# Kernel optimization log

Measured on AMD Instinct MI355X. Metric: run time of the kernel, lower is better.

## Reference

```python
import jax, jax.numpy as jnp
import numpy as np

NEG_INF = -1e30

def _pool_unpool(x, k):
    # x: [B, C, H, W]. Non-overlapping max pool with window k (floor-mode,
    # matching torch MaxPool2d default), then MaxUnpool: scatter the pooled max
    # back to its argmax location within each window, zeros elsewhere.
    B, C, H, W = x.shape
    Hc, Wc = (H // k) * k, (W // k) * k  # cropped region covered by windows
    xc = x[:, :, :Hc, :Wc]
    # reshape into windows: [B, C, H/k, k, W/k, k] -> [B, C, H/k, W/k, k*k]
    xw = xc.reshape(B, C, Hc // k, k, Wc // k, k).transpose(0, 1, 2, 4, 3, 5)
    xw = xw.reshape(B, C, Hc // k, Wc // k, k * k)
    mx = jnp.max(xw, axis=-1, keepdims=True)
    am = jnp.argmax(xw, axis=-1)  # first max index, matches torch tie-breaking
    onehot = (jnp.arange(k * k) == am[..., None])
    yw = jnp.where(onehot, mx, jnp.zeros_like(mx))
    yc = yw.reshape(B, C, Hc // k, Wc // k, k, k).transpose(0, 1, 2, 4, 3, 5)
    yc = yc.reshape(B, C, Hc, Wc)
    # output_size=size in torch unpool -> pad uncovered border with zeros
    return jnp.pad(yc, ((0, 0), (0, 0), (0, H - Hc), (0, W - Wc)))

def setup_inputs() -> dict:
    key = jax.random.key(0)
    x = jax.random.uniform(key, (16, 1, 1080, 1920), dtype=jnp.float32)
    return {"x": x}

def reference(x):
    k = 3
    x = _pool_unpool(x, k)
    x = _pool_unpool(x, k + 2)
    x = _pool_unpool(x, k + 3)
    return x
```

## Files before the change

kernel.cpp:

```cpp
#include <hip/hip_runtime.h>
#include <stdint.h>


#define IMG_H 1080
#define IMG_W 1920

template <int K>
__device__ __forceinline__ void stage(float (&v)[30], int cg, int cc) {
    constexpr int NW = 30 / K;
#pragma unroll
    for (int j = 0; j < NW; ++j) {
        float vm = v[j * K];
#pragma unroll
        for (int rr = 1; rr < K; ++rr) vm = fmaxf(vm, v[j * K + rr]);
        float M = vm;
#pragma unroll
        for (int q = 0; q < K; ++q) M = fmaxf(M, __shfl(vm, cg + q, 64));
        unsigned mask = 0u;
#pragma unroll
        for (int rr = 0; rr < K; ++rr)
            mask |= (v[j * K + rr] == M) ? (1u << rr) : 0u;
        unsigned comb = 0u, pre = 0u;
#pragma unroll
        for (int q = 0; q < K; ++q) {
            const unsigned mq = (unsigned)__shfl((int)mask, cg + q, 64);
            comb |= mq;
            pre |= (q < cc) ? mq : 0u;
        }
        const int R = __ffs(comb) - 1;
        const bool win = ((mask >> R) & 1u) != 0u && ((pre >> R) & 1u) == 0u;
#pragma unroll
        for (int rr = 0; rr < K; ++rr)
            v[j * K + rr] = (win && rr == R) ? M : 0.0f;
    }
}

__global__ __launch_bounds__(256, 6) void pooling_nms_kernel(
    const float* __restrict__ x, float* __restrict__ out) {
    const int t = threadIdx.x;
    const int w = t >> 6;
    const int lane = t & 63;
    const int c = (lane < 60) ? lane : 59;
    const int col0 = blockIdx.x * 240 + w * 60;
    const size_t base = (size_t)blockIdx.z * (IMG_H * (size_t)IMG_W) +
                        (size_t)(blockIdx.y * 30) * IMG_W + col0 + c;
    const float* src = x + base;
    float* dst = out + base;

    float v[30];
#pragma unroll
    for (int r = 0; r < 30; ++r) v[r] = src[(size_t)r * IMG_W];

    {
        const int cg = (c / 3) * 3;
        stage<3>(v, cg, c - cg);
    }
    {
        const int cg = (c / 5) * 5;
        stage<5>(v, cg, c - cg);
    }
    {
        const int cg = (c / 6) * 6;
        stage<6>(v, cg, c - cg);
    }

    if (lane < 60) {
#pragma unroll
        for (int r = 0; r < 30; ++r) dst[(size_t)r * IMG_W] = v[r];
    }
}

extern "C" void kernel_launch(void* const* d_in, const int* in_sizes, int n_in,
                              void* d_out, int out_size, void* d_ws, size_t ws_size,
                              hipStream_t stream) {
    const float* x = (const float*)d_in[0];
    float* out = (float*)d_out;
    dim3 grid(IMG_W / 240, IMG_H / 30, 16);
    pooling_nms_kernel<<<grid, 256, 0, stream>>>(x, out);
}
```

Before: 241.7 us.

## Stage tile through LDS with direct global-to-LDS 16-byte loads and float4 stores

Global reads now go straight into a shared-memory tile through the global_load_lds builtin, using 16-byte transfers in row-contiguous chunks instead of per-thread strided 4-byte loads. Each thread then reads its column from LDS, runs the three pool/unpool stages in registers, and writes results back to LDS. The tile is then stored to global memory as float4. The aim is wider, better-coalesced memory transactions. In exchange it adds two block barriers and about 30 KB of LDS per block, which may lower occupancy, and the min-blocks launch bound is dropped.

```diff
diff --git a/kernel.cpp b/kernel.cpp
--- a/kernel.cpp
+++ b/kernel.cpp
@@ -4,6 +4,13 @@
 
 #define IMG_H 1080
 #define IMG_W 1920
+#define TH 30
+#define TW 240
+#define LSTRIDE 256
+#define NTHREADS 256
+
+#define GPTR(p) ((const __attribute__((address_space(1))) void*)(p))
+#define LPTR(p) ((__attribute__((address_space(3))) void*)(p))
 
 template <int K>
 __device__ __forceinline__ void stage(float (&v)[30], int cg, int cc) {
@@ -35,21 +42,32 @@
     }
 }
 
-__global__ __launch_bounds__(256, 6) void pooling_nms_kernel(
+__global__ __launch_bounds__(NTHREADS) void pooling_nms_kernel(
     const float* __restrict__ x, float* __restrict__ out) {
+    __shared__ float tile[TH * LSTRIDE];
+
     const int t = threadIdx.x;
     const int w = t >> 6;
     const int lane = t & 63;
     const int c = (lane < 60) ? lane : 59;
-    const int col0 = blockIdx.x * 240 + w * 60;
+
     const size_t base = (size_t)blockIdx.z * (IMG_H * (size_t)IMG_W) +
-                        (size_t)(blockIdx.y * 30) * IMG_W + col0 + c;
+                        (size_t)(blockIdx.y * TH) * IMG_W + blockIdx.x * TW;
     const float* src = x + base;
     float* dst = out + base;
 
+    if (lane < 60) {
+        for (int r = w; r < TH; r += 4)
+            __builtin_amdgcn_global_load_lds(
+                GPTR(src + (size_t)r * IMG_W + lane * 4),
+                LPTR(&tile[r * LSTRIDE + lane * 4]), 16, 0, 0);
+    }
+    __syncthreads();
+
+    const int colw = 60 * w + c;
     float v[30];
 #pragma unroll
-    for (int r = 0; r < 30; ++r) v[r] = src[(size_t)r * IMG_W];
+    for (int r = 0; r < TH; ++r) v[r] = tile[r * LSTRIDE + colw];
 
     {
         const int cg = (c / 3) * 3;
@@ -66,7 +84,16 @@
 
     if (lane < 60) {
 #pragma unroll
-        for (int r = 0; r < 30; ++r) dst[(size_t)r * IMG_W] = v[r];
+        for (int r = 0; r < TH; ++r) tile[r * LSTRIDE + colw] = v[r];
+    }
+    __syncthreads();
+
+    if (lane < 60) {
+        for (int r = w; r < TH; r += 4) {
+            const float4 val =
+                *reinterpret_cast<const float4*>(&tile[r * LSTRIDE + lane * 4]);
+            *reinterpret_cast<float4*>(dst + (size_t)r * IMG_W + lane * 4) = val;
+        }
     }
 }
 
@@ -75,6 +102,6 @@
                               hipStream_t stream) {
     const float* x = (const float*)d_in[0];
     float* out = (float*)d_out;
-    dim3 grid(IMG_W / 240, IMG_H / 30, 16);
-    pooling_nms_kernel<<<grid, 256, 0, stream>>>(x, out);
+    dim3 grid(IMG_W / TW, IMG_H / TH, 16);
+    pooling_nms_kernel<<<grid, NTHREADS, 0, stream>>>(x, out);
 }
```

After: 233.3 us. 3.5% less time.
